# Kernel tuning notes

Hardware: AMD Instinct MI355X
Metric: run time of the kernel (lower is better)

Reference implementation:

```python
import jax, jax.numpy as jnp
import numpy as np

E = 256; D = 512; A = 5; NS = 2048; NQ = 8192; NWAY = 5
_OTHERS = np.array([[j for j in range(A) if j != i] for i in range(A)])  # [A, A-1] indices of other agents
_ROWS = np.arange(A)[:, None]


def _ln(x, g, b, eps=1e-5):
    m = x.mean(-1, keepdims=True)
    v = ((x - m) ** 2).mean(-1, keepdims=True)
    return (x - m) * jax.lax.rsqrt(v + eps) * g + b


def _mha(x, in_w, in_b, out_w, out_b, h, mask=None):
    # torch nn.MultiheadAttention (batch_first) self-attention. in_w: [3E,E], out_w: [E,E]
    B, S, Em = x.shape
    hd = Em // h
    qkv = x @ in_w.T + in_b
    q, k, v = jnp.split(qkv, 3, axis=-1)
    q = q.reshape(B, S, h, hd).transpose(0, 2, 1, 3) * (1.0 / np.sqrt(hd))
    k = k.reshape(B, S, h, hd).transpose(0, 2, 1, 3)
    v = v.reshape(B, S, h, hd).transpose(0, 2, 1, 3)
    s = jnp.einsum('bhqd,bhkd->bhqk', q, k)
    if mask is not None:
        s = jnp.where(mask, s, jnp.asarray(-1e9, s.dtype))
    a = jax.nn.softmax(s, axis=-1)
    o = jnp.einsum('bhqk,bhkd->bhqd', a, v).transpose(0, 2, 1, 3).reshape(B, S, Em)
    return o @ out_w.T + out_b


def _forward(support_x, support_y, query_x, n_way, fe0_w1, fe0_b1, fe0_g1, fe0_be1, fe0_w2, fe0_b2, fe0_g2, fe0_be2, fe1_w1, fe1_b1, fe1_g, fe1_be, fe1_w2, fe1_b2, fe2_w1, fe2_b1, fe2_w2, fe2_b2, fe2_g, fe2_be, fe3_w1, fe3_b1, fe3_w2, fe3_b2, fe3_g, fe3_be, fe4_w1, fe4_b1, fe4_w2, fe4_b2, fe4_w3, fe4_b3, msg_enc_w, msg_enc_b, agg_in_w, agg_in_b, agg_out_w, agg_out_b, proc_w1, proc_b1, proc_w2, proc_b2, internal_state, proto_in_w, proto_in_b, proto_out_w, proto_out_b, cls_w1, cls_b1, cls_w2, cls_b2, cls_w3, cls_b3, comm_w, f_w1, f_b1, f_w2, f_b2, f_w3, f_b3):
    # --- per-agent-type feature extractors (eval mode: dropout off) ---
    def fe0(x):
        h = jax.nn.relu(_ln(x @ fe0_w1 + fe0_b1, fe0_g1, fe0_be1))
        return jax.nn.relu(_ln(h @ fe0_w2 + fe0_b2, fe0_g2, fe0_be2))
    def fe1(x):
        h = jax.nn.relu(_ln(x @ fe1_w1 + fe1_b1, fe1_g, fe1_be))
        return jnp.tanh(h @ fe1_w2 + fe1_b2)
    def fe2(x):
        h = jax.nn.relu(x @ fe2_w1 + fe2_b1)
        return jax.nn.relu(_ln(h @ fe2_w2 + fe2_b2, fe2_g, fe2_be))
    def fe3(x):
        h = jax.nn.relu(x @ fe3_w1 + fe3_b1)
        return jax.nn.sigmoid(_ln(h @ fe3_w2 + fe3_b2, fe3_g, fe3_be))
    def fe4(x):
        h = jax.nn.relu(x @ fe4_w1 + fe4_b1)
        h = jax.nn.relu(h @ fe4_w2 + fe4_b2)
        return h @ fe4_w3 + fe4_b3
    feats_s = jnp.stack([fe0(support_x), fe1(support_x), fe2(support_x), fe3(support_x), fe4(support_x)])  # [A,NS,E]
    feats_q = jnp.stack([fe0(query_x), fe1(query_x), fe2(query_x), fe3(query_x), fe4(query_x)])            # [A,NQ,E]

    # --- one communication round: generate -> weight -> MHA-aggregate -> MLP-process ---
    agent_state = feats_s.mean(1) + internal_state                                         # [A,E]
    messages = jnp.tanh(jnp.einsum('ae,aef->af', agent_state, msg_enc_w) + msg_enc_b)      # [A,E]
    wgt = jax.nn.softmax(comm_w, axis=-1)                                                  # [A,A]
    msgs = messages[_OTHERS] * wgt[_ROWS, _OTHERS][..., None]                              # [A,A-1,E]
    def agg_one(m, iw, ib, ow, ob):
        return _mha(m[None], iw, ib, ow, ob, 4)[0].mean(0)
    agg = jax.vmap(agg_one)(msgs, agg_in_w, agg_in_b, agg_out_w, agg_out_b)                # [A,E]
    comb = internal_state + agg
    hh = jax.nn.relu(jnp.einsum('ae,aef->af', comb, proc_w1) + proc_b1)
    ck = jnp.einsum('ae,aef->af', hh, proc_w2) + proc_b2                                   # [A,E] communicated knowledge

    # --- class-masked prototype attention (equivalent to per-class MHA) + logits ---
    mask = support_y[:, None] == support_y[None, :]                                        # [NS,NS]
    counts = jax.ops.segment_sum(jnp.ones(support_y.shape, jnp.float32), support_y, num_segments=n_way)
    def head(fs, fq, cki, piw, pib, pw, pb, c1, c1b, c2, c2b, c3, c3b):
        att = _mha((fs + cki[None])[None], piw, pib, pw, pb, 2, mask[None, None])[0]       # [NS,E]
        psum = jax.ops.segment_sum(att, support_y, num_segments=n_way)
        protos = jnp.where(counts[:, None] > 0, psum / jnp.maximum(counts, 1.0)[:, None], 0.0)  # [n_way,E]
        eq = jnp.concatenate([fq, jnp.broadcast_to(cki, fq.shape)], axis=-1)               # [NQ,2E]
        d2 = (fq * fq).sum(-1, keepdims=True) + (protos * protos).sum(-1)[None, :] - 2.0 * (fq @ protos.T)
        dist = jnp.sqrt(jnp.maximum(d2, 1e-12))                                            # cdist
        c = jax.nn.relu(eq @ c1 + c1b)
        c = jax.nn.relu(c @ c2 + c2b)
        conf = c @ c3 + c3b                                                                # [NQ,1]
        return -dist + conf * 0.1
    logits = jax.vmap(head)(feats_s, feats_q, ck, proto_in_w, proto_in_b, proto_out_w, proto_out_b, cls_w1, cls_b1, cls_w2, cls_b2, cls_w3, cls_b3)  # [A,NQ,n_way]

    # --- decision fusion over concatenated per-agent query features ---
    qcat = feats_q.transpose(1, 0, 2).reshape(NQ, A * E)
    fh = jax.nn.relu(qcat @ f_w1 + f_b1)
    fh = jax.nn.relu(fh @ f_w2 + f_b2)
    fused = fh @ f_w3 + f_b3                                                               # [NQ,1]
    return logits, fused


def setup_inputs() -> dict:
    key = jax.random.key(0)
    ks = iter(jax.random.split(key, 80))
    def rn(shape, scale=1.0):
        return (jax.random.normal(next(ks), shape) * scale).astype(jnp.float32)
    def lin(shape, fan):
        return rn(shape, 1.0 / np.sqrt(fan))
    z = lambda s: jnp.zeros(s, jnp.float32)
    o = lambda s: jnp.ones(s, jnp.float32)
    inp = {}
    inp['support_x'] = rn((NS, D))
    inp['support_y'] = jax.random.randint(next(ks), (NS,), 0, NWAY, dtype=jnp.int32)
    inp['query_x'] = rn((NQ, D))
    inp['n_way'] = NWAY
    inp['fe0_w1'] = lin((D, 2 * E), D); inp['fe0_b1'] = z((2 * E,)); inp['fe0_g1'] = o((2 * E,)); inp['fe0_be1'] = z((2 * E,))
    inp['fe0_w2'] = lin((2 * E, E), 2 * E); inp['fe0_b2'] = z((E,)); inp['fe0_g2'] = o((E,)); inp['fe0_be2'] = z((E,))
    inp['fe1_w1'] = lin((D, E), D); inp['fe1_b1'] = z((E,)); inp['fe1_g'] = o((E,)); inp['fe1_be'] = z((E,))
    inp['fe1_w2'] = lin((E, E), E); inp['fe1_b2'] = z((E,))
    inp['fe2_w1'] = lin((D, 3 * E), D); inp['fe2_b1'] = z((3 * E,))
    inp['fe2_w2'] = lin((3 * E, E), 3 * E); inp['fe2_b2'] = z((E,)); inp['fe2_g'] = o((E,)); inp['fe2_be'] = z((E,))
    inp['fe3_w1'] = lin((D, E), D); inp['fe3_b1'] = z((E,))
    inp['fe3_w2'] = lin((E, E), E); inp['fe3_b2'] = z((E,)); inp['fe3_g'] = o((E,)); inp['fe3_be'] = z((E,))
    inp['fe4_w1'] = lin((D, 2 * E), D); inp['fe4_b1'] = z((2 * E,))
    inp['fe4_w2'] = lin((2 * E, E), 2 * E); inp['fe4_b2'] = z((E,))
    inp['fe4_w3'] = lin((E, E), E); inp['fe4_b3'] = z((E,))
    inp['msg_enc_w'] = lin((A, E, E), E); inp['msg_enc_b'] = z((A, E))
    inp['agg_in_w'] = lin((A, 3 * E, E), E); inp['agg_in_b'] = z((A, 3 * E))
    inp['agg_out_w'] = lin((A, E, E), E); inp['agg_out_b'] = z((A, E))
    inp['proc_w1'] = lin((A, E, E), E); inp['proc_b1'] = z((A, E))
    inp['proc_w2'] = lin((A, E, E), E); inp['proc_b2'] = z((A, E))
    inp['internal_state'] = rn((A, E), 0.01)
    inp['proto_in_w'] = lin((A, 3 * E, E), E); inp['proto_in_b'] = z((A, 3 * E))
    inp['proto_out_w'] = lin((A, E, E), E); inp['proto_out_b'] = z((A, E))
    inp['cls_w1'] = lin((A, 2 * E, E), 2 * E); inp['cls_b1'] = z((A, E))
    inp['cls_w2'] = lin((A, E, E // 2), E); inp['cls_b2'] = z((A, E // 2))
    inp['cls_w3'] = lin((A, E // 2, 1), E // 2); inp['cls_b3'] = z((A, 1))
    inp['comm_w'] = (jnp.eye(A) * 0.5 + 0.1).astype(jnp.float32)
    inp['f_w1'] = lin((A * E, E), A * E); inp['f_b1'] = z((E,))
    inp['f_w2'] = lin((E, E // 2), E); inp['f_b2'] = z((E // 2,))
    inp['f_w3'] = lin((E // 2, 1), E // 2); inp['f_b3'] = z((1,))
    return inp


def reference(support_x, support_y, query_x, n_way, fe0_w1, fe0_b1, fe0_g1, fe0_be1, fe0_w2, fe0_b2, fe0_g2, fe0_be2, fe1_w1, fe1_b1, fe1_g, fe1_be, fe1_w2, fe1_b2, fe2_w1, fe2_b1, fe2_w2, fe2_b2, fe2_g, fe2_be, fe3_w1, fe3_b1, fe3_w2, fe3_b2, fe3_g, fe3_be, fe4_w1, fe4_b1, fe4_w2, fe4_b2, fe4_w3, fe4_b3, msg_enc_w, msg_enc_b, agg_in_w, agg_in_b, agg_out_w, agg_out_b, proc_w1, proc_b1, proc_w2, proc_b2, internal_state, proto_in_w, proto_in_b, proto_out_w, proto_out_b, cls_w1, cls_b1, cls_w2, cls_b2, cls_w3, cls_b3, comm_w, f_w1, f_b1, f_w2, f_b2, f_w3, f_b3):
    return _forward(support_x, support_y, query_x, n_way, fe0_w1, fe0_b1, fe0_g1, fe0_be1, fe0_w2, fe0_b2, fe0_g2, fe0_be2, fe1_w1, fe1_b1, fe1_g, fe1_be, fe1_w2, fe1_b2, fe2_w1, fe2_b1, fe2_w2, fe2_b2, fe2_g, fe2_be, fe3_w1, fe3_b1, fe3_w2, fe3_b2, fe3_g, fe3_be, fe4_w1, fe4_b1, fe4_w2, fe4_b2, fe4_w3, fe4_b3, msg_enc_w, msg_enc_b, agg_in_w, agg_in_b, agg_out_w, agg_out_b, proc_w1, proc_b1, proc_w2, proc_b2, internal_state, proto_in_w, proto_in_b, proto_out_w, proto_out_b, cls_w1, cls_b1, cls_w2, cls_b2, cls_w3, cls_b3, comm_w, f_w1, f_b1, f_w2, f_b2, f_w3, f_b3)
```

## Files before the change

kernel.cpp:

```cpp
#include <hip/hip_runtime.h>
#include <hip/hip_bf16.h>

typedef __hip_bfloat16 bf16;
typedef short s8v __attribute__((ext_vector_type(8)));
typedef short s4v __attribute__((ext_vector_type(4)));
typedef float f4v __attribute__((ext_vector_type(4)));

#define A_  5
#define D_  512
#define E_  256
#define NS_ 2048
#define NQ_ 8192
#define NM_ 10240
#define NWAY_ 5
#define QSCALE 0.088388347648318447f
#define FSTR ((size_t)NM_ * E_)

__device__ inline float ldw(const void* p, size_t i, int f32) {
  return f32 ? ((const float*)p)[i] : __bfloat162float(((const bf16*)p)[i]);
}
template<bool DYN>
__device__ inline float ldT(const void* p, size_t i, int f32) {
  if (DYN) return ldw(p, i, f32);
  return ((const float*)p)[i];
}

__device__ inline short f2bf(float v) {
  union { float f; unsigned u; } x; x.f = v;
  unsigned r = x.u + 0x7fffu + ((x.u >> 16) & 1u);
  return (short)(r >> 16);
}
__device__ inline float bf2f(short s) {
  union { unsigned u; float f; } x; x.u = ((unsigned)(unsigned short)s) << 16;
  return x.f;
}

struct Ptrs { const void* p[64]; int sz[64]; };

__global__ void probe_k(Ptrs P, int* flags) {
  int b = blockIdx.x, lane = threadIdx.x;
  if (b == 1 || b == 3) { if (lane == 0) flags[b] = 0; return; }
  const bf16* t = (const bf16*)P.p[b];
  int n = P.sz[b];
  int K = (n >> 1) < 64 ? (n >> 1) : 64;
  bool big = false, eNZ = false, oNZ = false;
  if (lane < K) {
    float e = __bfloat162float(t[2 * lane]);
    float o = __bfloat162float(t[2 * lane + 1]);
    big = !(fabsf(e) <= 1e3f);
    eNZ = (e != 0.f); oNZ = (o != 0.f);
  }
  unsigned long long bb = __ballot(big), eb = __ballot(eNZ), ob = __ballot(oNZ);
  if (lane == 0) flags[b] = (bb != 0ull || (eb == 0ull && ob != 0ull)) ? 1 : 0;
}

__global__ void classidx_k(const int* __restrict__ y, int* __restrict__ idx,
                           int* __restrict__ cnt, int* __restrict__ cstart) {
  __shared__ int sc[NWAY_];
  int tid = threadIdx.x;
  if (tid < NWAY_) sc[tid] = 0;
  __syncthreads();
  for (int i = tid; i < NS_; i += 256) {
    int c = y[i];
    int pos = atomicAdd(&sc[c], 1);
    idx[c * NS_ + pos] = i;
  }
  __syncthreads();
  if (tid < NWAY_) cnt[tid] = sc[tid];
  if (tid == 0) { int s = 0; for (int q = 0; q < NWAY_; ++q) { cstart[q] = s; s += sc[q]; } }
}

__global__ void xcopy_k(const void* __restrict__ sx, const void* __restrict__ qx,
                        short* __restrict__ XC, const int* __restrict__ flags) {
  size_t i = ((size_t)blockIdx.x * 256 + threadIdx.x) * 4;
  const size_t SN = (size_t)NS_ * 512;
  if (i < SN) {
    int f = flags[0];
    #pragma unroll
    for (int q = 0; q < 4; ++q) XC[i + q] = f2bf(ldw(sx, i + q, f));
  } else {
    int f = flags[2];
    size_t j = i - SN;
    #pragma unroll
    for (int q = 0; q < 4; ++q) XC[i + q] = f2bf(ldw(qx, j + q, f));
  }
}

__global__ void wcat_k(Ptrs P, short* __restrict__ Wcat, float* __restrict__ bcat,
                       const int* __restrict__ flags) {
  int n = blockIdx.x * 256 + threadIdx.x;
  int k = blockIdx.y;
  int iw, ib, nl, Nloc;
  if (n < 512)       { iw = 4;  ib = 5;  nl = n;        Nloc = 512; }
  else if (n < 768)  { iw = 12; ib = 13; nl = n - 512;  Nloc = 256; }
  else if (n < 1536) { iw = 18; ib = 19; nl = n - 768;  Nloc = 768; }
  else if (n < 1792) { iw = 24; ib = 25; nl = n - 1536; Nloc = 256; }
  else               { iw = 30; ib = 31; nl = n - 1792; Nloc = 512; }
  Wcat[(size_t)n * 512 + k] = f2bf(ldw(P.p[iw], (size_t)k * Nloc + nl, flags[iw]));
  if (k == 0) bcat[n] = ldw(P.p[ib], nl, flags[ib]);
}

__global__ void wcls_k(const void* __restrict__ cw1, const void* __restrict__ fw1,
                       short* __restrict__ B2, const int* __restrict__ flags) {
  int n = blockIdx.x, a = blockIdx.y, k = threadIdx.x;
  float v;
  if (n < 256) v = ldw(cw1, ((size_t)a * 512 + k) * 256 + n, flags[51]);
  else v = ldw(fw1, ((size_t)(a * 256 + k)) * 256 + (n - 256), flags[58]);
  B2[((size_t)a * 512 + n) * 256 + k] = f2bf(v);
}

#define LSTR 40
template<int AMODE, int BMODE, bool DYNBIAS, bool TRB, int ACT, bool ACCUM,
         bool KSPLIT = false, bool OUTBF16 = false, bool DOMAP = false>
__global__ __launch_bounds__(256) void gemm_k(
    const void* __restrict__ A, int lda,
    const void* __restrict__ B, int ldb, size_t offB,
    const void* __restrict__ bias, size_t offBias,
    float* __restrict__ C, int ldc,
    int M, int N, int K, float alpha,
    int ia, int ib, int ibias, const int* __restrict__ flags,
    size_t sA, size_t sB, size_t sBias, size_t sC, size_t kstrideA,
    unsigned long long amap)
{
  const int fA = (AMODE == 1) ? flags[ia] : 1;
  const int fB = (BMODE == 1) ? flags[ib] : 1;
  const int fBi = DYNBIAS ? flags[ibias] : 1;
  const size_t zA = (size_t)blockIdx.z * sA;
  const size_t zB = offB + (size_t)blockIdx.z * sB;
  const size_t zBias = offBias + (size_t)blockIdx.z * sBias;
  float* Cz = C + (size_t)blockIdx.z * sC;
  bf16* Cz16 = (bf16*)C + (size_t)blockIdx.z * sC;
  __shared__ short As[128 * LSTR];
  __shared__ short Bs[128 * LSTR];
  const int tid = threadIdx.x;
  const int bm = blockIdx.y * 128, bn = blockIdx.x * 128;
  const int lane = tid & 63, wid = tid >> 6;
  const int lm = lane & 15, quad = lane >> 4;
  const int wy = (wid >> 1) * 64, wx = (wid & 1) * 64;
  f4v acc[4][4];
  #pragma unroll
  for (int i = 0; i < 4; ++i)
    #pragma unroll
    for (int j = 0; j < 4; ++j) acc[i][j] = (f4v)(0.f);

  const int am = tid >> 1, ah = (tid & 1) * 16;

  s8v a_s0, a_s1;
  float a_f[16];
  s8v b_s0, b_s1;
  float b_f[16];
  short b_h[16];

  auto loadA = [&](int k0) {
    int kk = k0 + ah;
    size_t base;
    if (KSPLIT) base = zA + (size_t)(kk >> 8) * kstrideA + (size_t)(bm + am) * lda + (kk & 255);
    else base = zA + (size_t)(bm + am) * lda + kk;
    if constexpr (AMODE == 2) {
      const bf16* ap = (const bf16*)A + base;
      a_s0 = *(const s8v*)ap;
      a_s1 = *(const s8v*)(ap + 8);
    } else {
      if (fA) {
        const float4* src = (const float4*)((const float*)A + base);
        #pragma unroll
        for (int q = 0; q < 4; ++q) {
          float4 v = src[q];
          a_f[q*4] = v.x; a_f[q*4+1] = v.y; a_f[q*4+2] = v.z; a_f[q*4+3] = v.w;
        }
      } else {
        #pragma unroll
        for (int q = 0; q < 16; ++q) a_f[q] = ldw(A, base + q, 0);
      }
    }
  };
  auto storeA = [&]() {
    if constexpr (AMODE == 2) {
      *(s8v*)&As[am * LSTR + ah] = a_s0;
      *(s8v*)&As[am * LSTR + ah + 8] = a_s1;
    } else {
      short tmp[16];
      #pragma unroll
      for (int q = 0; q < 16; ++q) tmp[q] = f2bf(a_f[q]);
      s4v* dst = (s4v*)&As[am * LSTR + ah];
      #pragma unroll
      for (int q = 0; q < 4; ++q) dst[q] = *(s4v*)&tmp[q*4];
    }
  };
  auto loadB = [&](int k0) {
    if constexpr (TRB) {
      int n = tid >> 1, h = (tid & 1) * 16;
      size_t base = zB + (size_t)(bn + n) * ldb + k0 + h;
      if constexpr (BMODE == 2) {
        const bf16* bp = (const bf16*)B + base;
        b_s0 = *(const s8v*)bp;
        b_s1 = *(const s8v*)(bp + 8);
      } else {
        if (fB) {
          const float4* src = (const float4*)((const float*)B + base);
          #pragma unroll
          for (int q = 0; q < 4; ++q) {
            float4 v = src[q];
            b_f[q*4] = v.x; b_f[q*4+1] = v.y; b_f[q*4+2] = v.z; b_f[q*4+3] = v.w;
          }
        } else {
          #pragma unroll
          for (int q = 0; q < 16; ++q) b_f[q] = ldw(B, base + q, 0);
        }
      }
    } else {
      int n = tid & 127, kk2 = (tid >> 7) * 16;
      #pragma unroll
      for (int j = 0; j < 16; ++j) {
        size_t bi = zB + (size_t)(k0 + kk2 + j) * ldb + bn + n;
        if constexpr (BMODE == 2) b_h[j] = ((const short*)B)[bi];
        else b_f[j] = ldT<BMODE == 1>(B, bi, fB);
      }
    }
  };
  auto storeB = [&]() {
    if constexpr (TRB) {
      int n = tid >> 1, h = (tid & 1) * 16;
      if constexpr (BMODE == 2) {
        *(s8v*)&Bs[n * LSTR + h] = b_s0;
        *(s8v*)&Bs[n * LSTR + h + 8] = b_s1;
      } else {
        short tmp[16];
        #pragma unroll
        for (int q = 0; q < 16; ++q) tmp[q] = f2bf(b_f[q]);
        s4v* dst = (s4v*)&Bs[n * LSTR + h];
        #pragma unroll
        for (int q = 0; q < 4; ++q) dst[q] = *(s4v*)&tmp[q*4];
      }
    } else {
      int n = tid & 127, kk2 = (tid >> 7) * 16;
      short tmp[16];
      #pragma unroll
      for (int j = 0; j < 16; ++j) tmp[j] = (BMODE == 2) ? b_h[j] : f2bf(b_f[j]);
      s4v* dst = (s4v*)&Bs[n * LSTR + kk2];
      #pragma unroll
      for (int q = 0; q < 4; ++q) dst[q] = *(s4v*)&tmp[q*4];
    }
  };

  loadA(0);
  loadB(0);
  for (int k0 = 0; k0 < K; k0 += 32) {
    storeA();
    storeB();
    __syncthreads();
    if (k0 + 32 < K) { loadA(k0 + 32); loadB(k0 + 32); }
    s8v af[4], bfr[4];
    #pragma unroll
    for (int mi = 0; mi < 4; ++mi)
      af[mi] = *(const s8v*)&As[(wy + mi*16 + lm) * LSTR + quad * 8];
    #pragma unroll
    for (int ni = 0; ni < 4; ++ni)
      bfr[ni] = *(const s8v*)&Bs[(wx + ni*16 + lm) * LSTR + quad * 8];
    #pragma unroll
    for (int mi = 0; mi < 4; ++mi)
      #pragma unroll
      for (int ni = 0; ni < 4; ++ni)
        acc[mi][ni] = __builtin_amdgcn_mfma_f32_16x16x32_bf16(af[mi], bfr[ni], acc[mi][ni], 0, 0, 0);
    __syncthreads();
  }
  const int actc = DOMAP ? (int)((amap >> ((bn >> 7) * 2)) & 3ULL) : ACT;
  #pragma unroll
  for (int mi = 0; mi < 4; ++mi) {
    #pragma unroll
    for (int r = 0; r < 4; ++r) {
      int row = bm + wy + mi*16 + quad*4 + r;
      #pragma unroll
      for (int ni = 0; ni < 4; ++ni) {
        int col = bn + wx + ni*16 + lm;
        float v = acc[mi][ni][r] * alpha;
        if (ACCUM) v += Cz[(size_t)row * ldc + col];
        if (bias) v += ldT<DYNBIAS>(bias, zBias + col, fBi);
        if (actc == 1) v = fmaxf(v, 0.f);
        else if (actc == 2) v = tanhf(v);
        else if (actc == 3) v = 1.f / (1.f + expf(-v));
        if (OUTBF16) Cz16[(size_t)row * ldc + col] = __float2bfloat16(v);
        else Cz[(size_t)row * ldc + col] = v;
      }
    }
  }
}

template<int AMODE, int BMODE, bool DYNBIAS, bool TRB, int ACT, bool ACCUM,
         bool KSPLIT = false, bool OUTBF16 = false, bool DOMAP = false>
static void gemm(hipStream_t s, const void* A, int lda, const void* B, int ldb, size_t offB,
                 const void* bias, size_t offBias, float* C, int ldc, int M, int N, int K,
                 float alpha, int ia, int ib, int ibias, const int* flags,
                 int batch = 1, size_t sA = 0, size_t sB = 0, size_t sBias = 0, size_t sC = 0,
                 size_t kstrideA = 0, unsigned long long amap = 0) {
  dim3 g(N / 128, M / 128, batch), b(256);
  gemm_k<AMODE, BMODE, DYNBIAS, TRB, ACT, ACCUM, KSPLIT, OUTBF16, DOMAP><<<g, b, 0, s>>>(
      A, lda, B, ldb, offB, bias, offBias, C, ldc, M, N, K, alpha, ia, ib, ibias, flags,
      sA, sB, sBias, sC, kstrideA, amap);
}

template<int ACT, bool INBF, bool OUTBF>
__global__ __launch_bounds__(256) void ln_k(const void* __restrict__ X, const void* __restrict__ g,
                                            const void* __restrict__ be, void* __restrict__ Y,
                                            int W, int ldx, int ldy,
                                            int ig, int ibe, const int* __restrict__ flags) {
  const int fG = flags[ig], fBe = flags[ibe];
  int row = blockIdx.x;
  const float* xf = (const float*)X + (size_t)row * ldx;
  const bf16* xb = (const bf16*)X + (size_t)row * ldx;
  float* yf = (float*)Y + (size_t)row * ldy;
  bf16* yb = (bf16*)Y + (size_t)row * ldy;
  __shared__ float red[256];
  int tid = threadIdx.x;
  float s1 = 0.f, s2 = 0.f;
  for (int i = tid; i < W; i += 256) {
    float v = INBF ? __bfloat162float(xb[i]) : xf[i];
    s1 += v; s2 += v * v;
  }
  red[tid] = s1; __syncthreads();
  for (int o = 128; o > 0; o >>= 1) { if (tid < o) red[tid] += red[tid + o]; __syncthreads(); }
  float mean = red[0] / W; __syncthreads();
  red[tid] = s2; __syncthreads();
  for (int o = 128; o > 0; o >>= 1) { if (tid < o) red[tid] += red[tid + o]; __syncthreads(); }
  float var = fmaxf(red[0] / W - mean * mean, 0.f);
  float rstd = rsqrtf(var + 1e-5f);
  for (int i = tid; i < W; i += 256) {
    float x = INBF ? __bfloat162float(xb[i]) : xf[i];
    float v = (x - mean) * rstd * ldw(g, i, fG) + ldw(be, i, fBe);
    if (ACT == 1) v = fmaxf(v, 0.f);
    else if (ACT == 3) v = 1.f / (1.f + expf(-v));
    if (OUTBF) yb[i] = __float2bfloat16(v);
    else yf[i] = v;
  }
}

__global__ void statepart_k(const short* __restrict__ featsC, float* __restrict__ part) {
  int a = blockIdx.x, g = blockIdx.y, e = threadIdx.x;
  const short* p = featsC + (size_t)a * FSTR + ((size_t)g * 128) * E_ + e;
  float s = 0.f;
  for (int n = 0; n < 128; ++n) s += bf2f(p[(size_t)n * E_]);
  part[((size_t)a * 16 + g) * E_ + e] = s;
}

__global__ void statecomb_k(const float* __restrict__ part, const void* __restrict__ internal,
                            float* __restrict__ state, const int* __restrict__ flags) {
  int a = blockIdx.x, e = threadIdx.x;
  float s = 0.f;
  for (int g = 0; g < 16; ++g) s += part[((size_t)a * 16 + g) * E_ + e];
  state[a * E_ + e] = s * (1.f / NS_) + ldw(internal, (size_t)a * E_ + e, flags[46]);
}

__global__ void mvpart_k(const float* __restrict__ x, const void* __restrict__ W, int iw,
                         float* __restrict__ part, const int* __restrict__ flags) {
  int a = blockIdx.x, g = blockIdx.y, f = threadIdx.x;
  const int fW = flags[iw];
  float s = 0.f;
  size_t wb = (size_t)a * E_ * E_ + f;
  for (int e = g * 32; e < g * 32 + 32; ++e)
    s += x[a * E_ + e] * ldw(W, wb + (size_t)e * E_, fW);
  part[((size_t)a * 8 + g) * E_ + f] = s;
}

template<int ACT>
__global__ void mvcomb_k(const float* __restrict__ part, const void* __restrict__ b, int ibb,
                         float* __restrict__ y, const int* __restrict__ flags) {
  int a = blockIdx.x, f = threadIdx.x;
  float s = 0.f;
  for (int g = 0; g < 8; ++g) s += part[((size_t)a * 8 + g) * E_ + f];
  s += ldw(b, (size_t)a * E_ + f, flags[ibb]);
  if (ACT == 1) s = fmaxf(s, 0.f);
  else if (ACT == 2) s = tanhf(s);
  y[a * E_ + f] = s;
}

__device__ inline float wave_sum64(float v) {
  for (int o = 32; o > 0; o >>= 1) v += __shfl_down(v, o);
  return v;
}

__global__ __launch_bounds__(256) void qkvcomm_k(const float* __restrict__ msg,
                                                 const void* __restrict__ comm_w,
                                                 const void* __restrict__ in_w,
                                                 const void* __restrict__ in_b,
                                                 float* __restrict__ qkvc,
                                                 const int* __restrict__ flags) {
  const int fCW = flags[57], fIW = flags[38], fIB = flags[39];
  int gw = blockIdx.x * 4 + (threadIdx.x >> 6);
  int a = gw / 768, f = gw % 768;
  int lane = threadIdx.x & 63;
  float w[5]; float mx = -1e30f;
  for (int j = 0; j < 5; ++j) { w[j] = ldw(comm_w, a * 5 + j, fCW); mx = fmaxf(mx, w[j]); }
  float sum = 0.f;
  for (int j = 0; j < 5; ++j) { w[j] = __expf(w[j] - mx); sum += w[j]; }
  for (int j = 0; j < 5; ++j) w[j] /= sum;
  int others[4]; { int c = 0; for (int j = 0; j < 5; ++j) if (j != a) others[c++] = j; }
  int e0 = lane * 4;
  float4 wv;
  size_t b = (size_t)a * 768 * E_ + (size_t)f * E_ + e0;
  if (fIW) wv = *(const float4*)((const float*)in_w + b);
  else wv = make_float4(ldw(in_w, b, 0), ldw(in_w, b + 1, 0), ldw(in_w, b + 2, 0), ldw(in_w, b + 3, 0));
  float acc[4];
  #pragma unroll
  for (int t = 0; t < 4; ++t) {
    const float4 mv = *(const float4*)(msg + others[t] * E_ + e0);
    acc[t] = mv.x * wv.x + mv.y * wv.y + mv.z * wv.z + mv.w * wv.w;
  }
  #pragma unroll
  for (int t = 0; t < 4; ++t) acc[t] = wave_sum64(acc[t]);
  if (lane == 0) {
    float bb = ldw(in_b, (size_t)a * 768 + f, fIB);
    #pragma unroll
    for (int t = 0; t < 4; ++t)
      qkvc[((size_t)a * 4 + t) * 768 + f] = acc[t] * w[others[t]] + bb;
  }
}

__global__ __launch_bounds__(256) void attn4_k(const float* __restrict__ qkvc,
                                               float* __restrict__ obar) {
  int a = blockIdx.x, tid = threadIdx.x;
  __shared__ float qkv[4][768];
  __shared__ float attw[4][16];
  for (int i = tid; i < 4 * 768; i += 256) qkv[i / 768][i % 768] = qkvc[(size_t)a * 4 * 768 + i];
  __syncthreads();
  if (tid < 16) {
    int h = tid >> 2, t = tid & 3;
    float sc[4]; float mx = -1e30f;
    for (int t2 = 0; t2 < 4; ++t2) {
      float s = 0.f;
      for (int d = 0; d < 64; ++d) s += qkv[t][h * 64 + d] * qkv[t2][256 + h * 64 + d];
      sc[t2] = s * 0.125f; mx = fmaxf(mx, sc[t2]);
    }
    float ss = 0.f;
    for (int t2 = 0; t2 < 4; ++t2) { sc[t2] = __expf(sc[t2] - mx); ss += sc[t2]; }
    for (int t2 = 0; t2 < 4; ++t2) attw[h][t * 4 + t2] = sc[t2] / ss;
  }
  __syncthreads();
  {
    int e = tid, h = e >> 6;
    float s = 0.f;
    for (int t = 0; t < 4; ++t)
      for (int t2 = 0; t2 < 4; ++t2)
        s += attw[h][t * 4 + t2] * qkv[t2][512 + e];
    obar[a * E_ + e] = s * 0.25f;
  }
}

__global__ __launch_bounds__(256) void combproj_k(const float* __restrict__ obar,
                                                  const void* __restrict__ ow,
                                                  const void* __restrict__ ob,
                                                  const void* __restrict__ internal,
                                                  float* __restrict__ comb,
                                                  const int* __restrict__ flags) {
  const int fOW = flags[40], fOB = flags[41], fIN = flags[46];
  int gw = blockIdx.x * 4 + (threadIdx.x >> 6);
  int a = gw >> 8, f = gw & 255;
  int lane = threadIdx.x & 63;
  int e0 = lane * 4;
  float4 wv;
  size_t b = (size_t)a * E_ * E_ + (size_t)f * E_ + e0;
  if (fOW) wv = *(const float4*)((const float*)ow + b);
  else wv = make_float4(ldw(ow, b, 0), ldw(ow, b + 1, 0), ldw(ow, b + 2, 0), ldw(ow, b + 3, 0));
  const float4 ov = *(const float4*)(obar + a * E_ + e0);
  float s = wave_sum64(ov.x * wv.x + ov.y * wv.y + ov.z * wv.z + ov.w * wv.w);
  if (lane == 0)
    comb[a * E_ + f] = ldw(internal, (size_t)a * E_ + f, fIN) + s + ldw(ob, (size_t)a * E_ + f, fOB);
}

__global__ __launch_bounds__(256) void ckb_k(const float* __restrict__ ck,
                                             const void* __restrict__ in_w,
                                             const void* __restrict__ in_b,
                                             float* __restrict__ ckb,
                                             const int* __restrict__ flags) {
  const int fW = flags[47], fB = flags[48];
  int gw = blockIdx.x * 4 + (threadIdx.x >> 6);
  int a = gw / 768, f = gw % 768;
  int lane = threadIdx.x & 63;
  int e0 = lane * 4;
  float4 wv;
  size_t b = (size_t)a * 768 * E_ + (size_t)f * E_ + e0;
  if (fW) wv = *(const float4*)((const float*)in_w + b);
  else wv = make_float4(ldw(in_w, b, 0), ldw(in_w, b + 1, 0), ldw(in_w, b + 2, 0), ldw(in_w, b + 3, 0));
  const float4 cv = *(const float4*)(ck + a * E_ + e0);
  float s = wave_sum64(cv.x * wv.x + cv.y * wv.y + cv.z * wv.z + cv.w * wv.w);
  if (lane == 0) ckb[(size_t)a * 768 + f] = s + ldw(in_b, (size_t)a * 768 + f, fB);
}

#define LS 136
__device__ inline void stage64x128(const short* __restrict__ qkv, const int* __restrict__ myidx,
                                   int row0, int n, int ho, short* dst) {
  int t = threadIdx.x;
  int r = t >> 2, c0 = (t & 3) * 32;
  int rr = row0 + r;
  s8v v0 = (s8v)(short)0, v1 = v0, v2 = v0, v3 = v0;
  if (rr < n) {
    const s8v* s = (const s8v*)(qkv + (size_t)myidx[rr] * 768 + ho + c0);
    v0 = s[0]; v1 = s[1]; v2 = s[2]; v3 = s[3];
  }
  s8v* d = (s8v*)&dst[r * LS + c0];
  d[0] = v0; d[1] = v1; d[2] = v2; d[3] = v3;
}

__global__ __launch_bounds__(256) void attn_stats_k(
    const short* __restrict__ qkv_all, const int* __restrict__ idx,
    const int* __restrict__ cnt, const int* __restrict__ cstart,
    float* __restrict__ ml)
{
  int c = blockIdx.x, z = blockIdx.z, a = z >> 1, h = z & 1;
  int n = cnt[c];
  int r0 = blockIdx.y * 64;
  if (r0 >= n) return;
  const short* qkv = qkv_all + (size_t)a * NS_ * 768;
  const int* myidx = idx + c * NS_;
  __shared__ short Qs[64 * LS];
  __shared__ short Ks[64 * LS];
  __shared__ float Mw[4][64], Lw[4][64];
  int tid = threadIdx.x, lane = tid & 63, wid = tid >> 6;
  int lm = lane & 15, quad = lane >> 4;
  stage64x128(qkv, myidx, r0, n, h * 128, Qs);
  float m_run[16], l_run[16];
  #pragma unroll
  for (int i = 0; i < 16; ++i) { m_run[i] = -3e38f; l_run[i] = 0.f; }
  for (int j0 = 0; j0 < n; j0 += 64) {
    __syncthreads();
    stage64x128(qkv, myidx, j0, n, 256 + h * 128, Ks);
    __syncthreads();
    f4v acc[4];
    #pragma unroll
    for (int mi = 0; mi < 4; ++mi) acc[mi] = (f4v)(0.f);
    #pragma unroll
    for (int kc = 0; kc < 4; ++kc) {
      s8v bfr = *(const s8v*)&Ks[(wid * 16 + lm) * LS + kc * 32 + quad * 8];
      #pragma unroll
      for (int mi = 0; mi < 4; ++mi) {
        s8v af = *(const s8v*)&Qs[(mi * 16 + lm) * LS + kc * 32 + quad * 8];
        acc[mi] = __builtin_amdgcn_mfma_f32_16x16x32_bf16(af, bfr, acc[mi], 0, 0, 0);
      }
    }
    int col = j0 + wid * 16 + lm;
    bool cv = col < n;
    #pragma unroll
    for (int mi = 0; mi < 4; ++mi) {
      #pragma unroll
      for (int r = 0; r < 4; ++r) {
        float s = cv ? acc[mi][r] * QSCALE : -3e38f;
        float m = s;
        m = fmaxf(m, __shfl_xor(m, 1));
        m = fmaxf(m, __shfl_xor(m, 2));
        m = fmaxf(m, __shfl_xor(m, 4));
        m = fmaxf(m, __shfl_xor(m, 8));
        float p = cv ? __expf(s - m) : 0.f;
        p += __shfl_xor(p, 1); p += __shfl_xor(p, 2);
        p += __shfl_xor(p, 4); p += __shfl_xor(p, 8);
        int ri = mi * 4 + r;
        float mo = m_run[ri];
        float mn = fmaxf(mo, m);
        l_run[ri] = l_run[ri] * __expf(mo - mn) + p * __expf(m - mn);
        m_run[ri] = mn;
      }
    }
  }
  if (lm == 0) {
    #pragma unroll
    for (int mi = 0; mi < 4; ++mi)
      #pragma unroll
      for (int r = 0; r < 4; ++r) {
        int row = mi * 16 + quad * 4 + r;
        Mw[wid][row] = m_run[mi * 4 + r];
        Lw[wid][row] = l_run[mi * 4 + r];
      }
  }
  __syncthreads();
  if (tid < 64 && r0 + tid < n) {
    float m = fmaxf(fmaxf(Mw[0][tid], Mw[1][tid]), fmaxf(Mw[2][tid], Mw[3][tid]));
    float l = Lw[0][tid] * __expf(Mw[0][tid] - m) + Lw[1][tid] * __expf(Mw[1][tid] - m)
            + Lw[2][tid] * __expf(Mw[2][tid] - m) + Lw[3][tid] * __expf(Mw[3][tid] - m);
    size_t p = (size_t)z * NS_ + cstart[c] + r0 + tid;
    ml[p * 2] = m; ml[p * 2 + 1] = l;
  }
}

__global__ __launch_bounds__(256) void attn_colsum_k(
    const short* __restrict__ qkv_all, const int* __restrict__ idx,
    const int* __restrict__ cnt, const int* __restrict__ cstart,
    const float* __restrict__ ml, float* __restrict__ colsum)
{
  int c = blockIdx.x, z = blockIdx.z, a = z >> 1, h = z & 1;
  int n = cnt[c];
  int j0 = blockIdx.y * 64;
  if (j0 >= n) return;
  const short* qkv = qkv_all + (size_t)a * NS_ * 768;
  const int* myidx = idx + c * NS_;
  __shared__ short Qs[64 * LS];
  __shared__ short Ks[64 * LS];
  __shared__ float Msm[64], Lsm[64];
  int tid = threadIdx.x, lane = tid & 63, wid = tid >> 6;
  int lm = lane & 15, quad = lane >> 4;
  stage64x128(qkv, myidx, j0, n, 256 + h * 128, Ks);
  float ca = 0.f;
  for (int i0 = 0; i0 < n; i0 += 64) {
    __syncthreads();
    stage64x128(qkv, myidx, i0, n, h * 128, Qs);
    if (tid < 64) {
      int gi = i0 + tid;
      if (gi < n) {
        size_t p = (size_t)z * NS_ + cstart[c] + gi;
        Msm[tid] = ml[p * 2]; Lsm[tid] = ml[p * 2 + 1];
      } else { Msm[tid] = 0.f; Lsm[tid] = 1.f; }
    }
    __syncthreads();
    f4v acc[4];
    #pragma unroll
    for (int mi = 0; mi < 4; ++mi) acc[mi] = (f4v)(0.f);
    #pragma unroll
    for (int kc = 0; kc < 4; ++kc) {
      s8v bfr = *(const s8v*)&Ks[(wid * 16 + lm) * LS + kc * 32 + quad * 8];
      #pragma unroll
      for (int mi = 0; mi < 4; ++mi) {
        s8v af = *(const s8v*)&Qs[(mi * 16 + lm) * LS + kc * 32 + quad * 8];
        acc[mi] = __builtin_amdgcn_mfma_f32_16x16x32_bf16(af, bfr, acc[mi], 0, 0, 0);
      }
    }
    #pragma unroll
    for (int mi = 0; mi < 4; ++mi) {
      #pragma unroll
      for (int r = 0; r < 4; ++r) {
        int lrow = mi * 16 + quad * 4 + r;
        int gi = i0 + lrow;
        if (gi < n) {
          float m = Msm[lrow];
          float invl = 1.f / Lsm[lrow];
          ca += __expf(acc[mi][r] * QSCALE - m) * invl;
        }
      }
    }
  }
  ca += __shfl_xor(ca, 16);
  ca += __shfl_xor(ca, 32);
  int col = j0 + wid * 16 + lm;
  if (quad == 0 && col < n)
    colsum[(size_t)z * NS_ + cstart[c] + col] = ca;
}

#define PCH 8
__global__ __launch_bounds__(1024) void proto_reduce_k(
    const short* __restrict__ qkv_all, const int* __restrict__ idx,
    const int* __restrict__ cnt, const int* __restrict__ cstart,
    const float* __restrict__ colsum, float* __restrict__ proto_pre) {
  int c = blockIdx.x, a = blockIdx.y;
  int n = cnt[c];
  int tid = threadIdx.x, lane = tid & 63, wid = tid >> 6;
  int h = lane >> 5;
  int e0 = lane * 4;
  const short* qkv = qkv_all + (size_t)a * NS_ * 768 + 512;
  const float* csum = colsum + (size_t)(a * 2 + h) * NS_ + cstart[c];
  const int* myidx = idx + c * NS_;
  float a0 = 0.f, a1 = 0.f, a2 = 0.f, a3 = 0.f;
  for (int k = wid; k < n; k += 16) {
    float w = csum[k];
    const s4v v = *(const s4v*)(qkv + (size_t)myidx[k] * 768 + e0);
    a0 += w * bf2f(v[0]); a1 += w * bf2f(v[1]);
    a2 += w * bf2f(v[2]); a3 += w * bf2f(v[3]);
  }
  __shared__ float red[16][E_];
  *(float4*)&red[wid][e0] = make_float4(a0, a1, a2, a3);
  __syncthreads();
  if (tid < E_) {
    float s = 0.f;
    #pragma unroll
    for (int wdx = 0; wdx < 16; ++wdx) s += red[wdx][tid];
    proto_pre[((size_t)a * NWAY_ + c) * E_ + tid] = (n > 0) ? s / (float)n : 0.f;
  }
}

__global__ void proto_outproj_k(const float* __restrict__ proto_pre, const void* __restrict__ ow,
                                const void* __restrict__ ob, const int* __restrict__ cnt,
                                float* __restrict__ protos_all, const int* __restrict__ flags) {
  int c = blockIdx.x, a = blockIdx.y, e = threadIdx.x;
  const int fW = flags[49], fB = flags[50];
  __shared__ float pp[E_];
  pp[e] = proto_pre[((size_t)a * NWAY_ + c) * E_ + e];
  __syncthreads();
  size_t wb = (size_t)a * E_ * E_ + (size_t)e * E_;
  float s = 0.f;
  for (int k = 0; k < E_; ++k) s += pp[k] * ldw(ow, wb + k, fW);
  float v = s + ldw(ob, (size_t)a * E_ + e, fB);
  protos_all[((size_t)a * NWAY_ + c) * E_ + e] = (cnt[c] > 0) ? v : 0.f;
}

__global__ void bias2_k(const float* __restrict__ ck, const void* __restrict__ w1,
                        const void* __restrict__ b1, float* __restrict__ biascat2,
                        const int* __restrict__ flags) {
  const int fW = flags[51], fB = flags[52];
  int a = blockIdx.x, n = threadIdx.x;
  __shared__ float c[E_];
  c[n] = ck[a * E_ + n]; __syncthreads();
  size_t wbase = (size_t)a * 2 * E_ * E_ + (size_t)E_ * E_ + n;
  float s = 0.f;
  for (int k = 0; k < E_; ++k) s += c[k] * ldw(w1, wbase + (size_t)k * E_, fW);
  biascat2[(size_t)a * 512 + n] = s + ldw(b1, (size_t)a * E_ + n, fB);
  biascat2[(size_t)a * 512 + 256 + n] = 0.f;
}

__global__ void fcomb_k(const short* __restrict__ U, const void* __restrict__ b1,
                        short* __restrict__ fh1, const int* __restrict__ flags) {
  int i = blockIdx.x, n = threadIdx.x;
  const int fB = flags[59];
  float s = 0.f;
  #pragma unroll
  for (int a = 0; a < A_; ++a)
    s += bf2f(U[((size_t)a * NQ_ + i) * 512 + 256 + n]);
  s += ldw(b1, n, fB);
  fh1[(size_t)i * 256 + n] = f2bf(fmaxf(s, 0.f));
}

__global__ __launch_bounds__(64) void logits_k(const short* __restrict__ fqbase,
                                               const float* __restrict__ protos_all,
                                               const bf16* __restrict__ c2all,
                                               const void* __restrict__ w3,
                                               const void* __restrict__ b3,
                                               float* __restrict__ out,
                                               const int* __restrict__ flags) {
  const int fW = flags[55], fB = flags[56];
  int i = blockIdx.x, a = blockIdx.y, lane = threadIdx.x;
  const short* fq = fqbase + (size_t)a * FSTR + (size_t)i * E_ + lane * 4;
  const float* protos = protos_all + (size_t)a * NWAY_ * E_;
  const bf16* c2 = c2all + ((size_t)a * NQ_ + i) * 128;
  s4v xv4 = *(const s4v*)fq;
  float x0 = bf2f(xv4[0]), x1 = bf2f(xv4[1]), x2 = bf2f(xv4[2]), x3 = bf2f(xv4[3]);
  float qq = wave_sum64(x0 * x0 + x1 * x1 + x2 * x2 + x3 * x3);
  float cpart = __bfloat162float(c2[lane * 2]) * ldw(w3, (size_t)a * 128 + lane * 2, fW) +
                __bfloat162float(c2[lane * 2 + 1]) * ldw(w3, (size_t)a * 128 + lane * 2 + 1, fW);
  float conf = wave_sum64(cpart);
  if (lane == 0) conf += ldw(b3, a, fB);
  for (int c = 0; c < NWAY_; ++c) {
    float4 pv = ((const float4*)(protos + c * E_))[lane];
    float dt = wave_sum64(x0 * pv.x + x1 * pv.y + x2 * pv.z + x3 * pv.w);
    float pp = wave_sum64(pv.x * pv.x + pv.y * pv.y + pv.z * pv.z + pv.w * pv.w);
    if (lane == 0) {
      float d2 = fmaxf(qq + pp - 2.f * dt, 1e-12f);
      out[((size_t)a * NQ_ + i) * NWAY_ + c] = -sqrtf(d2) + 0.1f * conf;
    }
  }
}

__global__ __launch_bounds__(64) void fused_k(const float* __restrict__ h2, const void* __restrict__ w3,
                                              const void* __restrict__ b3, float* __restrict__ out,
                                              const int* __restrict__ flags) {
  const int fW = flags[62], fB = flags[63];
  int i = blockIdx.x, lane = threadIdx.x;
  float s = h2[(size_t)i * 128 + lane * 2] * ldw(w3, lane * 2, fW) +
            h2[(size_t)i * 128 + lane * 2 + 1] * ldw(w3, lane * 2 + 1, fW);
  s = wave_sum64(s);
  if (lane == 0) out[i] = s + ldw(b3, 0, fB);
}

extern "C" void kernel_launch(void* const* d_in, const int* in_sizes, int n_in,
                              void* d_out, int out_size, void* d_ws, size_t ws_size,
                              hipStream_t stream) {
  (void)out_size; (void)ws_size;
  #define P(i) ((const void*)d_in[i])
  const int* support_y = (const int*)d_in[1];
  float* out = (float*)d_out;

  int* flags = (int*)d_ws;
  char* base = (char*)d_ws + 256;
  short* featsC = (short*)base;
  char* R = base + (size_t)A_ * FSTR * 2;
  short* t1cat   = (short*)R;
  short* qkv_all = (short*)R;
  short* U       = (short*)(R + (size_t)15728640);
  short* fh1     = (short*)R;
  float* fh2     = (float*)(R + (size_t)8388608);
  char* XCR = R + (size_t)57671680;
  short* XC   = (short*)XCR;
  short* tmp2 = (short*)XCR;
  short* b4   = (short*)(XCR + (size_t)NM_ * 256 * 2);
  short* clsC2_all = (short*)XCR;
  char* S = XCR + (size_t)10485760;
  float* state      = (float*)S;
  float* msg        = state + A_ * E_;
  float* ck         = msg + A_ * E_;
  float* protos_all = ck + A_ * E_;
  float* biascat2   = protos_all + A_ * NWAY_ * E_;
  float* ml         = biascat2 + A_ * 512;
  float* colsum     = ml + (size_t)A_ * 2 * NS_ * 2;
  float* proto_pre  = colsum + (size_t)A_ * 2 * NS_;
  int*   idx        = (int*)(proto_pre + A_ * NWAY_ * E_);
  int*   cnt        = idx + NWAY_ * NS_;
  int*   cstart     = cnt + NWAY_;
  float* statepart  = (float*)(cstart + NWAY_ + 3);
  float* mvp        = statepart + A_ * 16 * E_;
  float* qkvc       = mvp + A_ * 8 * E_;
  float* obar       = qkvc + A_ * 4 * 768;
  float* comb       = obar + A_ * E_;
  float* hh         = comb + A_ * E_;
  float* ckb        = hh + A_ * E_;
  float* ppart      = ckb + A_ * 768;
  float* bcat       = ppart + (size_t)A_ * NWAY_ * PCH * E_;
  short* Wcat       = (short*)(bcat + 2304);
  short* Bcat2      = Wcat + (size_t)2304 * 512;

  const short* fq_base = featsC + (size_t)NS_ * E_;

  Ptrs ps;
  for (int i = 0; i < 64; ++i) {
    ps.p[i] = (i < n_in) ? d_in[i] : nullptr;
    ps.sz[i] = (i < n_in) ? in_sizes[i] : 0;
  }
  probe_k<<<64, 64, 0, stream>>>(ps, flags);
  classidx_k<<<1, 256, 0, stream>>>(support_y, idx, cnt, cstart);
  xcopy_k<<<(NM_ * 512 / 4) / 256, 256, 0, stream>>>(P(0), P(2), XC, flags);
  wcat_k<<<dim3(9, 512), 256, 0, stream>>>(ps, Wcat, bcat, flags);
  wcls_k<<<dim3(512, A_), 256, 0, stream>>>(P(51), P(58), Bcat2, flags);

  gemm<2, 2, false, true, 0, false, false, true, true>(
      stream, XC, 512, Wcat, 512, 0, bcat, 0, (float*)t1cat, 2304,
      NM_, 2304, 512, 1.f, -1, -1, -1, flags, 1, 0, 0, 0, 0, 0, 0x555555000ULL);
  ln_k<1, true, true><<<NM_, 256, 0, stream>>>(t1cat, P(6), P(7), t1cat, 512, 2304, 2304, 6, 7, flags);
  gemm<2, 1, true, false, 0, false, false, true>(stream, t1cat, 2304, P(8), 256, 0, P(9), 0,
                                                 (float*)tmp2, 256, NM_, 256, 512, 1.f, -1, 8, 9, flags);
  ln_k<1, true, true><<<NM_, 256, 0, stream>>>(tmp2, P(10), P(11), featsC, 256, 256, 256, 10, 11, flags);
  ln_k<1, true, true><<<NM_, 256, 0, stream>>>(t1cat + 512, P(14), P(15), t1cat + 512, 256, 2304, 2304, 14, 15, flags);
  gemm<2, 1, true, false, 2, false, false, true>(stream, t1cat + 512, 2304, P(16), 256, 0, P(17), 0,
                                                 (float*)(featsC + FSTR), 256, NM_, 256, 256, 1.f, -1, 16, 17, flags);
  gemm<2, 1, true, false, 0, false, false, true>(stream, t1cat + 768, 2304, P(20), 256, 0, P(21), 0,
                                                 (float*)tmp2, 256, NM_, 256, 768, 1.f, -1, 20, 21, flags);
  ln_k<1, true, true><<<NM_, 256, 0, stream>>>(tmp2, P(22), P(23), featsC + 2 * FSTR, 256, 256, 256, 22, 23, flags);
  gemm<2, 1, true, false, 0, false, false, true>(stream, t1cat + 1536, 2304, P(26), 256, 0, P(27), 0,
                                                 (float*)tmp2, 256, NM_, 256, 256, 1.f, -1, 26, 27, flags);
  ln_k<3, true, true><<<NM_, 256, 0, stream>>>(tmp2, P(28), P(29), featsC + 3 * FSTR, 256, 256, 256, 28, 29, flags);
  gemm<2, 1, true, false, 1, false, false, true>(stream, t1cat + 1792, 2304, P(32), 256, 0, P(33), 0,
                                                 (float*)b4, 256, NM_, 256, 512, 1.f, -1, 32, 33, flags);
  gemm<2, 1, true, false, 0, false, false, true>(stream, b4, 256, P(34), 256, 0, P(35), 0,
                                                 (float*)(featsC + 4 * FSTR), 256, NM_, 256, 256, 1.f, -1, 34, 35, flags);

  statepart_k<<<dim3(A_, 16), 256, 0, stream>>>(featsC, statepart);
  statecomb_k<<<A_, 256, 0, stream>>>(statepart, P(46), state, flags);
  mvpart_k<<<dim3(A_, 8), 256, 0, stream>>>(state, P(36), 36, mvp, flags);
  mvcomb_k<2><<<A_, 256, 0, stream>>>(mvp, P(37), 37, msg, flags);
  qkvcomm_k<<<A_ * 768 / 4, 256, 0, stream>>>(msg, P(57), P(38), P(39), qkvc, flags);
  attn4_k<<<A_, 256, 0, stream>>>(qkvc, obar);
  combproj_k<<<A_ * E_ / 4, 256, 0, stream>>>(obar, P(40), P(41), P(46), comb, flags);
  mvpart_k<<<dim3(A_, 8), 256, 0, stream>>>(comb, P(42), 42, mvp, flags);
  mvcomb_k<1><<<A_, 256, 0, stream>>>(mvp, P(43), 43, hh, flags);
  mvpart_k<<<dim3(A_, 8), 256, 0, stream>>>(hh, P(44), 44, mvp, flags);
  mvcomb_k<0><<<A_, 256, 0, stream>>>(mvp, P(45), 45, ck, flags);

  ckb_k<<<A_ * 768 / 4, 256, 0, stream>>>(ck, P(47), P(48), ckb, flags);
  gemm<2, 1, false, true, 0, false, false, true>(stream, featsC, 256, P(47), 256, 0, ckb, 0,
                                    (float*)qkv_all, 768, NS_, 768, 256, 1.f, -1, 47, -1, flags,
                                    A_, FSTR, (size_t)3 * E_ * E_, (size_t)768, (size_t)NS_ * 768);
  {
    dim3 g(NWAY_, NS_ / 64, A_ * 2);
    attn_stats_k<<<g, 256, 0, stream>>>(qkv_all, idx, cnt, cstart, ml);
    attn_colsum_k<<<g, 256, 0, stream>>>(qkv_all, idx, cnt, cstart, ml, colsum);
  }
  proto_reduce_k<<<dim3(NWAY_, A_), 1024, 0, stream>>>(qkv_all, idx, cnt, cstart, colsum, proto_pre);
  proto_outproj_k<<<dim3(NWAY_, A_), 256, 0, stream>>>(proto_pre, P(49), P(50), cnt, protos_all, flags);
  bias2_k<<<A_, 256, 0, stream>>>(ck, P(51), P(52), biascat2, flags);

  gemm<2, 2, false, true, 0, false, false, true, true>(
      stream, fq_base, 256, Bcat2, 256, 0, biascat2, 0, (float*)U, 512,
      NQ_, 512, 256, 1.f, -1, -1, -1, flags,
      A_, FSTR, (size_t)512 * 256, (size_t)512, (size_t)NQ_ * 512, 0, 0x5ULL);
  fcomb_k<<<NQ_, 256, 0, stream>>>(U, P(59), fh1, flags);

  gemm<2, 1, true, false, 1, false, false, true>(stream, U, 512, P(53), 128, 0,
                                     P(54), 0, (float*)clsC2_all, 128, NQ_, 128, 256, 1.f, -1, 53, 54, flags,
                                     A_, (size_t)NQ_ * 512, (size_t)E_ * 128, (size_t)128, (size_t)NQ_ * 128);
  logits_k<<<dim3(NQ_, A_), 64, 0, stream>>>(fq_base, protos_all, (const bf16*)clsC2_all, P(55), P(56), out, flags);

  gemm<2, 1, true, false, 1, false>(stream, fh1, 256, P(60), 128, 0, P(61), 0, fh2, 128, NQ_, 128, 256, 1.f, -1, 60, 61, flags);
  fused_k<<<NQ_, 64, 0, stream>>>(fh2, P(62), P(63), out + (size_t)A_ * NQ_ * NWAY_, flags);
}
```

Measured before the change: 915.1 us.

## Double-buffer GEMM LDS tiles and use direct global-to-LDS loads for bf16

The GEMM kernel now keeps two LDS buffers per operand, so the next K-tile is staged while MFMAs run on the current one, and only one barrier is needed per iteration. For bf16 operands (row-major A, transposed B) it issues global_load_lds 16-byte direct loads into an unpadded 32-stride LDS layout, skipping the register round trip. This doubles LDS use and drops the padding, which may cause bank conflicts on the fragment reads. It also relies on the barrier to cover completion of the async LDS loads.

```diff
diff --git a/kernel.cpp b/kernel.cpp
--- a/kernel.cpp
+++ b/kernel.cpp
@@ -33,6 +33,12 @@
 __device__ inline float bf2f(short s) {
   union { unsigned u; float f; } x; x.u = ((unsigned)(unsigned short)s) << 16;
   return x.f;
+}
+
+__device__ __forceinline__ void gload16(const void* g, void* l) {
+  __builtin_amdgcn_global_load_lds(
+      (const __attribute__((address_space(1))) unsigned int*)g,
+      (__attribute__((address_space(3))) unsigned int*)l, 16, 0, 0);
 }
 
 struct Ptrs { const void* p[64]; int sz[64]; };
@@ -122,6 +128,10 @@
     size_t sA, size_t sB, size_t sBias, size_t sC, size_t kstrideA,
     unsigned long long amap)
 {
+  constexpr bool GLA = (AMODE == 2) && !KSPLIT;
+  constexpr bool GLB = (BMODE == 2) && TRB;
+  constexpr int LSA = GLA ? 32 : LSTR;
+  constexpr int LSB = GLB ? 32 : LSTR;
   const int fA = (AMODE == 1) ? flags[ia] : 1;
   const int fB = (BMODE == 1) ? flags[ib] : 1;
   const int fBi = DYNBIAS ? flags[ibias] : 1;
@@ -130,8 +140,8 @@
   const size_t zBias = offBias + (size_t)blockIdx.z * sBias;
   float* Cz = C + (size_t)blockIdx.z * sC;
   bf16* Cz16 = (bf16*)C + (size_t)blockIdx.z * sC;
-  __shared__ short As[128 * LSTR];
-  __shared__ short Bs[128 * LSTR];
+  __shared__ short As[2][128 * LSA];
+  __shared__ short Bs[2][128 * LSB];
   const int tid = threadIdx.x;
   const int bm = blockIdx.y * 128, bn = blockIdx.x * 128;
   const int lane = tid & 63, wid = tid >> 6;
@@ -145,68 +155,66 @@
 
   const int am = tid >> 1, ah = (tid & 1) * 16;
 
-  s8v a_s0, a_s1;
   float a_f[16];
-  s8v b_s0, b_s1;
   float b_f[16];
   short b_h[16];
+
+  auto stageA_g = [&](int bsel, int k0) {
+    #pragma unroll
+    for (int q = 0; q < 2; ++q) {
+      int row = (wid * 2 + q) * 16 + (lane >> 2);
+      const bf16* src = (const bf16*)A + zA + (size_t)(bm + row) * lda + k0 + (lane & 3) * 8;
+      gload16(src, &As[bsel][(wid * 2 + q) * 512]);
+    }
+  };
+  auto stageB_g = [&](int bsel, int k0) {
+    #pragma unroll
+    for (int q = 0; q < 2; ++q) {
+      int row = (wid * 2 + q) * 16 + (lane >> 2);
+      const bf16* src = (const bf16*)B + zB + (size_t)(bn + row) * ldb + k0 + (lane & 3) * 8;
+      gload16(src, &Bs[bsel][(wid * 2 + q) * 512]);
+    }
+  };
 
   auto loadA = [&](int k0) {
     int kk = k0 + ah;
     size_t base;
     if (KSPLIT) base = zA + (size_t)(kk >> 8) * kstrideA + (size_t)(bm + am) * lda + (kk & 255);
     else base = zA + (size_t)(bm + am) * lda + kk;
-    if constexpr (AMODE == 2) {
-      const bf16* ap = (const bf16*)A + base;
-      a_s0 = *(const s8v*)ap;
-      a_s1 = *(const s8v*)(ap + 8);
+    if (fA) {
+      const float4* src = (const float4*)((const float*)A + base);
+      #pragma unroll
+      for (int q = 0; q < 4; ++q) {
+        float4 v = src[q];
+        a_f[q*4] = v.x; a_f[q*4+1] = v.y; a_f[q*4+2] = v.z; a_f[q*4+3] = v.w;
+      }
     } else {
-      if (fA) {
-        const float4* src = (const float4*)((const float*)A + base);
-        #pragma unroll
-        for (int q = 0; q < 4; ++q) {
-          float4 v = src[q];
-          a_f[q*4] = v.x; a_f[q*4+1] = v.y; a_f[q*4+2] = v.z; a_f[q*4+3] = v.w;
-        }
-      } else {
-        #pragma unroll
-        for (int q = 0; q < 16; ++q) a_f[q] = ldw(A, base + q, 0);
-      }
+      #pragma unroll
+      for (int q = 0; q < 16; ++q) a_f[q] = ldw(A, base + q, 0);
     }
   };
-  auto storeA = [&]() {
-    if constexpr (AMODE == 2) {
-      *(s8v*)&As[am * LSTR + ah] = a_s0;
-      *(s8v*)&As[am * LSTR + ah + 8] = a_s1;
-    } else {
-      short tmp[16];
-      #pragma unroll
-      for (int q = 0; q < 16; ++q) tmp[q] = f2bf(a_f[q]);
-      s4v* dst = (s4v*)&As[am * LSTR + ah];
-      #pragma unroll
-      for (int q = 0; q < 4; ++q) dst[q] = *(s4v*)&tmp[q*4];
-    }
+  auto storeA = [&](int bsel) {
+    short tmp[16];
+    #pragma unroll
+    for (int q = 0; q < 16; ++q) tmp[q] = f2bf(a_f[q]);
+    s4v* dst = (s4v*)&As[bsel][am * LSA + ah];
+    #pragma unroll
+    for (int q = 0; q < 4; ++q) dst[q] = *(s4v*)&tmp[q*4];
   };
   auto loadB = [&](int k0) {
     if constexpr (TRB) {
       int n = tid >> 1, h = (tid & 1) * 16;
       size_t base = zB + (size_t)(bn + n) * ldb + k0 + h;
-      if constexpr (BMODE == 2) {
-        const bf16* bp = (const bf16*)B + base;
-        b_s0 = *(const s8v*)bp;
-        b_s1 = *(const s8v*)(bp + 8);
+      if (fB) {
+        const float4* src = (const float4*)((const float*)B + base);
+        #pragma unroll
+        for (int q = 0; q < 4; ++q) {
+          float4 v = src[q];
+          b_f[q*4] = v.x; b_f[q*4+1] = v.y; b_f[q*4+2] = v.z; b_f[q*4+3] = v.w;
+        }
       } else {
-        if (fB) {
-          const float4* src = (const float4*)((const float*)B + base);
-          #pragma unroll
-          for (int q = 0; q < 4; ++q) {
-            float4 v = src[q];
-            b_f[q*4] = v.x; b_f[q*4+1] = v.y; b_f[q*4+2] = v.z; b_f[q*4+3] = v.w;
-          }
-        } else {
-          #pragma unroll
-          for (int q = 0; q < 16; ++q) b_f[q] = ldw(B, base + q, 0);
-        }
+        #pragma unroll
+        for (int q = 0; q < 16; ++q) b_f[q] = ldw(B, base + q, 0);
       }
     } else {
       int n = tid & 127, kk2 = (tid >> 7) * 16;
@@ -218,52 +226,57 @@
       }
     }
   };
-  auto storeB = [&]() {
+  auto storeB = [&](int bsel) {
     if constexpr (TRB) {
       int n = tid >> 1, h = (tid & 1) * 16;
-      if constexpr (BMODE == 2) {
-        *(s8v*)&Bs[n * LSTR + h] = b_s0;
-        *(s8v*)&Bs[n * LSTR + h + 8] = b_s1;
-      } else {
-        short tmp[16];
-        #pragma unroll
-        for (int q = 0; q < 16; ++q) tmp[q] = f2bf(b_f[q]);
-        s4v* dst = (s4v*)&Bs[n * LSTR + h];
-        #pragma unroll
-        for (int q = 0; q < 4; ++q) dst[q] = *(s4v*)&tmp[q*4];
-      }
+      short tmp[16];
+      #pragma unroll
+      for (int q = 0; q < 16; ++q) tmp[q] = f2bf(b_f[q]);
+      s4v* dst = (s4v*)&Bs[bsel][n * LSB + h];
+      #pragma unroll
+      for (int q = 0; q < 4; ++q) dst[q] = *(s4v*)&tmp[q*4];
     } else {
       int n = tid & 127, kk2 = (tid >> 7) * 16;
       short tmp[16];
       #pragma unroll
       for (int j = 0; j < 16; ++j) tmp[j] = (BMODE == 2) ? b_h[j] : f2bf(b_f[j]);
-      s4v* dst = (s4v*)&Bs[n * LSTR + kk2];
+      s4v* dst = (s4v*)&Bs[bsel][n * LSB + kk2];
       #pragma unroll
       for (int q = 0; q < 4; ++q) dst[q] = *(s4v*)&tmp[q*4];
     }
   };
 
-  loadA(0);
-  loadB(0);
+  if constexpr (GLA) stageA_g(0, 0); else { loadA(0); storeA(0); }
+  if constexpr (GLB) stageB_g(0, 0); else { loadB(0); storeB(0); }
+  __syncthreads();
+
+  int cur = 0;
   for (int k0 = 0; k0 < K; k0 += 32) {
-    storeA();
-    storeB();
-    __syncthreads();
-    if (k0 + 32 < K) { loadA(k0 + 32); loadB(k0 + 32); }
+    const bool more = (k0 + 32 < K);
+    if (more) {
+      if constexpr (GLA) stageA_g(cur ^ 1, k0 + 32); else loadA(k0 + 32);
+      if constexpr (GLB) stageB_g(cur ^ 1, k0 + 32); else loadB(k0 + 32);
+    }
     s8v af[4], bfr[4];
     #pragma unroll
     for (int mi = 0; mi < 4; ++mi)
-      af[mi] = *(const s8v*)&As[(wy + mi*16 + lm) * LSTR + quad * 8];
+      af[mi] = *(const s8v*)&As[cur][(wy + mi*16 + lm) * LSA + quad * 8];
     #pragma unroll
     for (int ni = 0; ni < 4; ++ni)
-      bfr[ni] = *(const s8v*)&Bs[(wx + ni*16 + lm) * LSTR + quad * 8];
+      bfr[ni] = *(const s8v*)&Bs[cur][(wx + ni*16 + lm) * LSB + quad * 8];
     #pragma unroll
     for (int mi = 0; mi < 4; ++mi)
       #pragma unroll
       for (int ni = 0; ni < 4; ++ni)
         acc[mi][ni] = __builtin_amdgcn_mfma_f32_16x16x32_bf16(af[mi], bfr[ni], acc[mi][ni], 0, 0, 0);
+    if (more) {
+      if constexpr (!GLA) storeA(cur ^ 1);
+      if constexpr (!GLB) storeB(cur ^ 1);
+    }
     __syncthreads();
-  }
+    cur ^= 1;
+  }
+
   const int actc = DOMAP ? (int)((amap >> ((bn >> 7) * 2)) & 3ULL) : ACT;
   #pragma unroll
   for (int mi = 0; mi < 4; ++mi) {
```

Result: no change. 932.9 us (+1.9%).
